# Performance work log

Measured on AMD Instinct MI355X. Metric: run time of the kernel, lower is better.

Reference implementation:

```python
import jax, jax.numpy as jnp
import numpy as np

N = 50000      # nodes
E = 1600000    # edges (avg degree 32)
D = 128        # node feature dim
C = 10         # classes
BN_EPS = 1e-5


def _w(k, shape, fan_in):
    lim = 1.0 / np.sqrt(fan_in)
    return jax.random.uniform(k, shape, jnp.float32, -lim, lim)


def setup_inputs() -> dict:
    key = jax.random.key(0)
    ks = jax.random.split(key, 16)
    inp = {}
    inp["x"] = jax.random.normal(ks[0], (N, D), jnp.float32)
    inp["edge_attr"] = jax.random.normal(ks[1], (E, 1), jnp.float32)
    inp["edge_index"] = jax.random.randint(ks[2], (2, E), 0, N)
    # edge-attr projection Linear(1, D) (D_n > D_e branch)
    inp["lin_w"] = _w(ks[3], (1, D), 1)
    inp["lin_b"] = jnp.zeros((D,), jnp.float32)
    # conv1 nn: MLP([D, D]) = Linear + ReLU + BatchNorm1d
    inp["w1"] = _w(ks[4], (D, D), D); inp["b1"] = jnp.zeros((D,)); inp["g1"] = jnp.ones((D,)); inp["be1"] = jnp.zeros((D,))
    # conv2 nn: MLP([D, 64])
    inp["w2"] = _w(ks[5], (D, 64), D); inp["b2"] = jnp.zeros((64,)); inp["g2"] = jnp.ones((64,)); inp["be2"] = jnp.zeros((64,))
    # lin1: MLP([D+64, 96])
    inp["w3"] = _w(ks[6], (D + 64, 96), D + 64); inp["b3"] = jnp.zeros((96,)); inp["g3"] = jnp.ones((96,)); inp["be3"] = jnp.zeros((96,))
    # mlp1: MLP([96, 96, C])
    inp["w4"] = _w(ks[7], (96, 96), 96); inp["b4"] = jnp.zeros((96,)); inp["g4"] = jnp.ones((96,)); inp["be4"] = jnp.zeros((96,))
    inp["w5"] = _w(ks[8], (96, C), 96); inp["b5"] = jnp.zeros((C,)); inp["g5"] = jnp.ones((C,)); inp["be5"] = jnp.zeros((C,))
    return inp


def _bn(h, g, b):
    # BatchNorm1d training-mode: batch statistics, biased variance
    m = h.mean(axis=0)
    v = h.var(axis=0)
    return g * (h - m) * jax.lax.rsqrt(v + BN_EPS) + b


def _mlp_layer(h, w, b, g, be):
    # nn.Sequential(Linear, ReLU, BatchNorm1d)
    return _bn(jax.nn.relu(h @ w + b), g, be)


def reference(x, edge_attr, edge_index, lin_w, lin_b,
              w1, b1, g1, be1, w2, b2, g2, be2,
              w3, b3, g3, be3, w4, b4, g4, be4,
              w5, b5, g5, be5):
    # project scalar edge features to node dim (D_n > D_e branch)
    e = edge_attr @ lin_w + lin_b  # [E, D]
    src, dst = edge_index[0], edge_index[1]

    def gine(h, w, b, g, be):
        # GINEConv (eps=0): nn(x_i + sum_j relu(x_j + e_ji))
        msg = jax.nn.relu(h[src] + e)                      # [E, D]
        aggr = jax.ops.segment_sum(msg, dst, num_segments=N)  # [N, D]
        return _mlp_layer(h + aggr, w, b, g, be)

    x1 = gine(x, w1, b1, g1, be1)    # [N, D]
    x2 = gine(x1, w2, b2, g2, be2)   # [N, 64]
    h = _mlp_layer(jnp.concatenate([x1, x2], axis=1), w3, b3, g3, be3)  # [N, 96]
    h = _mlp_layer(h, w4, b4, g4, be4)  # [N, 96]
    h = _mlp_layer(h, w5, b5, g5, be5)  # [N, C]
    return h
```

## Files before the change

kernel.cpp:

```cpp
#include <hip/hip_runtime.h>
#include <hip/hip_fp16.h>

static constexpr float BN_EPS = 1e-5f;

using half8 = __attribute__((ext_vector_type(8))) _Float16;
using f32x4 = __attribute__((ext_vector_type(4))) float;

__device__ __forceinline__ ushort f2h(float f) {
    return __half_as_ushort(__float2half(f));
}
__device__ __forceinline__ float2 h2f2(uint u) {
    __half2 h = *reinterpret_cast<__half2*>(&u);
    return __half22float2(h);
}
__device__ __forceinline__ float h2f1(ushort u) {
    __half h = *reinterpret_cast<__half*>(&u);
    return __half2float(h);
}

__global__ __launch_bounds__(256) void cvt_f16(
    const float* __restrict__ in, ushort* __restrict__ out, int n4)
{
    int i = blockIdx.x * 256 + threadIdx.x;
    const int stride = gridDim.x * 256;
    for (; i < n4; i += stride) {
        const float4 v = ((const float4*)in)[i];
        ushort4 u;
        u.x = f2h(v.x); u.y = f2h(v.y); u.z = f2h(v.z); u.w = f2h(v.w);
        ((ushort4*)out)[i] = u;
    }
}

__device__ __forceinline__ void pack_store(ushort* dst, int M, int k, int c, float v)
{
    const int kc = k >> 5, kk = k & 31, ct = c >> 4;
    const int lane = (c & 15) | ((kk >> 3) << 4);
    const int j = kk & 7;
    dst[((size_t)(kc * (M / 16) + ct) * 64 + lane) * 8 + j] = f2h(v);
}

__global__ __launch_bounds__(256) void pack_all(
    const float* __restrict__ w1, const float* __restrict__ w2,
    const float* __restrict__ w3, const float* __restrict__ w4,
    const float* __restrict__ w5, const float* __restrict__ b5,
    ushort* __restrict__ Wp, float* __restrict__ b5p, float* __restrict__ sums)
{
    int t = blockIdx.x * 256 + threadIdx.x;
    if (t < 16384) { pack_store(Wp, 128, t / 128, t % 128, w1[t]); return; }
    t -= 16384;
    if (t < 8192) { pack_store(Wp + 16384, 64, t / 64, t % 64, w2[t]); return; }
    t -= 8192;
    if (t < 18432) { pack_store(Wp + 24576, 96, t / 96, t % 96, w3[t]); return; }
    t -= 18432;
    if (t < 9216) { pack_store(Wp + 43008, 96, t / 96, t % 96, w4[t]); return; }
    t -= 9216;
    if (t < 1536) {
        const int k = t / 16, c = t % 16;
        pack_store(Wp + 52224, 16, k, c, (c < 10) ? w5[k * 10 + c] : 0.f);
        return;
    }
    t -= 1536;
    if (t < 16) { b5p[t] = (t < 10) ? b5[t] : 0.f; return; }
    t -= 16;
    if (t < 1280) sums[t] = 0.f;
}

__device__ inline int wave_incl_scan(int v, int lane)
{
#pragma unroll
    for (int s = 1; s < 64; s <<= 1) {
        const int t = __shfl_up(v, s, 64);
        if (lane >= s) v += t;
    }
    return v;
}

__global__ __launch_bounds__(1024) void scan1(
    const int* __restrict__ cnt, int* __restrict__ off, int* __restrict__ bsum, int n)
{
    __shared__ int wsum[16];
    const int tid = threadIdx.x, lane = tid & 63, wid = tid >> 6;
    const int i = blockIdx.x * 1024 + tid;
    const int v = (i < n) ? cnt[i] : 0;
    const int incl = wave_incl_scan(v, lane);
    if (lane == 63) wsum[wid] = incl;
    __syncthreads();
    if (wid == 0) {
        int wv = (lane < 16) ? wsum[lane] : 0;
        wv = wave_incl_scan(wv, lane);
        if (lane < 16) wsum[lane] = wv;
    }
    __syncthreads();
    const int excl = (wid > 0 ? wsum[wid - 1] : 0) + incl - v;
    if (i < n) off[i] = excl;
    if (tid == 1023) bsum[blockIdx.x] = wsum[15];
}

__global__ __launch_bounds__(64) void scan2(int* __restrict__ bsum, int nb)
{
    const int lane = threadIdx.x;
    int carry = 0;
    for (int base = 0; base < nb; base += 64) {
        const int idx = base + lane;
        const int v = (idx < nb) ? bsum[idx] : 0;
        const int incl = wave_incl_scan(v, lane);
        if (idx < nb) bsum[idx] = carry + incl - v;
        carry += __shfl(incl, 63, 64);
    }
}

__global__ __launch_bounds__(1024) void scan3(
    int* __restrict__ off, const int* __restrict__ bsum, int n)
{
    const int i = blockIdx.x * 1024 + threadIdx.x;
    if (i < n) off[i] += bsum[blockIdx.x];
}

__global__ __launch_bounds__(256) void hist_blocks(
    const int* __restrict__ dst, int* __restrict__ H, int E, int NB, int NBLK)
{
    __shared__ int h[512];
    for (int i = threadIdx.x; i < NB; i += 256) h[i] = 0;
    __syncthreads();
    const int chunk = (E + NBLK - 1) / NBLK;
    const int beg = blockIdx.x * chunk;
    const int end = min(beg + chunk, E);
    for (int i = beg + threadIdx.x; i < end; i += 256)
        atomicAdd(&h[dst[i] >> 7], 1);
    __syncthreads();
    for (int i = threadIdx.x; i < NB; i += 256)
        H[(size_t)i * NBLK + blockIdx.x] = h[i];
}

__global__ __launch_bounds__(256) void scatter_coarse(
    const int* __restrict__ src, const int* __restrict__ dst,
    const float* __restrict__ ea, const int* __restrict__ H,
    int2* __restrict__ tmp, int E, int NB, int NBLK)
{
    __shared__ int h[512];
    for (int i = threadIdx.x; i < NB; i += 256)
        h[i] = H[(size_t)i * NBLK + blockIdx.x];
    __syncthreads();
    const int chunk = (E + NBLK - 1) / NBLK;
    const int beg = blockIdx.x * chunk;
    const int end = min(beg + chunk, E);
    for (int i = beg + threadIdx.x; i < end; i += 256) {
        const int d = dst[i];
        const int pos = atomicAdd(&h[d >> 7], 1);
        tmp[pos] = make_int2(src[i] | ((d & 127) << 20), __float_as_int(ea[i]));
    }
}

__global__ __launch_bounds__(256) void fill_fine2(
    const int2* __restrict__ tmp, const int* __restrict__ H,
    int* __restrict__ off, uint* __restrict__ edges, int N, int E, int NBLK)
{
    __shared__ int cnt[128];
    __shared__ int wtot;
    const int b = blockIdx.x;
    const int base = b * 128;
    const int tid = threadIdx.x;
    const int lo = H[(size_t)b * NBLK];
    const int hi = (b + 1 < (int)gridDim.x) ? H[(size_t)(b + 1) * NBLK] : E;
    if (tid < 128) cnt[tid] = 0;
    __syncthreads();
    for (int i = lo + tid; i < hi; i += 256)
        atomicAdd(&cnt[(tmp[i].x >> 20) & 127], 1);
    __syncthreads();
    int excl = 0;
    if (tid < 128) {
        const int v = cnt[tid];
        const int incl = wave_incl_scan(v, tid & 63);
        if (tid == 63) wtot = incl;
        excl = incl - v;
    }
    __syncthreads();
    if (tid >= 64 && tid < 128) excl += wtot;
    if (tid < 128) {
        const int o = lo + excl;
        if (base + tid < N) off[base + tid] = o;
        cnt[tid] = o;
    }
    if (b == 0 && tid == 0) off[N] = E;
    __syncthreads();
    for (int i = lo + tid; i < hi; i += 256) {
        const int2 p = tmp[i];
        const int dl = (p.x >> 20) & 127;
        const int pos = atomicAdd(&cnt[dl], 1);
        edges[pos] = (uint)(p.x & 0xFFFF) | ((uint)f2h(__int_as_float(p.y)) << 16);
    }
}

template<bool AFF>
__global__ __launch_bounds__(256) void gine_aggr(
    const ushort* __restrict__ xh, const int* __restrict__ off,
    const uint* __restrict__ edges, const float* __restrict__ lw,
    const float* __restrict__ lb, const float* __restrict__ sc,
    const float* __restrict__ sh, ushort* __restrict__ outh, int N)
{
    const int q = threadIdx.x & 31;
    const int node = blockIdx.x * 8 + (threadIdx.x >> 5);
    if (node >= N) return;
    const float4 lw4 = ((const float4*)lw)[q];
    const float4 lb4 = ((const float4*)lb)[q];
    float4 sc4, sh4;
    if constexpr (AFF) {
        sc4 = ((const float4*)sc)[q];
        sh4 = ((const float4*)sh)[q];
    }
    float4 s;
    {
        const uint2 u = ((const uint2*)(xh + (size_t)node * 128))[q];
        float2 f0 = h2f2(u.x), f1 = h2f2(u.y);
        if constexpr (AFF) {
            f0.x = fmaf(f0.x, sc4.x, sh4.x); f0.y = fmaf(f0.y, sc4.y, sh4.y);
            f1.x = fmaf(f1.x, sc4.z, sh4.z); f1.y = fmaf(f1.y, sc4.w, sh4.w);
        }
        s.x = f0.x; s.y = f0.y; s.z = f1.x; s.w = f1.y;
    }

    auto acc1 = [&](uint e, uint2 u) {
        const float a = h2f1((ushort)(e >> 16));
        float2 f0 = h2f2(u.x), f1 = h2f2(u.y);
        if constexpr (AFF) {
            f0.x = fmaf(f0.x, sc4.x, sh4.x); f0.y = fmaf(f0.y, sc4.y, sh4.y);
            f1.x = fmaf(f1.x, sc4.z, sh4.z); f1.y = fmaf(f1.y, sc4.w, sh4.w);
        }
        s.x += fmaxf(fmaf(a, lw4.x, lb4.x) + f0.x, 0.f);
        s.y += fmaxf(fmaf(a, lw4.y, lb4.y) + f0.y, 0.f);
        s.z += fmaxf(fmaf(a, lw4.z, lb4.z) + f1.x, 0.f);
        s.w += fmaxf(fmaf(a, lw4.w, lb4.w) + f1.y, 0.f);
    };

    int p = off[node];
    const int pend = off[node + 1];
    for (; p + 8 <= pend; p += 8) {
        const uint e0 = edges[p + 0], e1 = edges[p + 1];
        const uint e2 = edges[p + 2], e3 = edges[p + 3];
        const uint e4 = edges[p + 4], e5 = edges[p + 5];
        const uint e6 = edges[p + 6], e7 = edges[p + 7];
        const uint2 u0 = ((const uint2*)(xh + (size_t)(e0 & 0xFFFFu) * 128))[q];
        const uint2 u1 = ((const uint2*)(xh + (size_t)(e1 & 0xFFFFu) * 128))[q];
        const uint2 u2 = ((const uint2*)(xh + (size_t)(e2 & 0xFFFFu) * 128))[q];
        const uint2 u3 = ((const uint2*)(xh + (size_t)(e3 & 0xFFFFu) * 128))[q];
        const uint2 u4 = ((const uint2*)(xh + (size_t)(e4 & 0xFFFFu) * 128))[q];
        const uint2 u5 = ((const uint2*)(xh + (size_t)(e5 & 0xFFFFu) * 128))[q];
        const uint2 u6 = ((const uint2*)(xh + (size_t)(e6 & 0xFFFFu) * 128))[q];
        const uint2 u7 = ((const uint2*)(xh + (size_t)(e7 & 0xFFFFu) * 128))[q];
        acc1(e0, u0); acc1(e1, u1); acc1(e2, u2); acc1(e3, u3);
        acc1(e4, u4); acc1(e5, u5); acc1(e6, u6); acc1(e7, u7);
    }
    for (; p < pend; ++p) {
        const uint e = edges[p];
        const uint2 u = ((const uint2*)(xh + (size_t)(e & 0xFFFFu) * 128))[q];
        acc1(e, u);
    }
    ushort4 o;
    o.x = f2h(s.x); o.y = f2h(s.y); o.z = f2h(s.z); o.w = f2h(s.w);
    ((ushort4*)(outh + (size_t)node * 128))[q] = o;
}

__device__ __forceinline__ half8 affine_h8(
    half8 a, const float* __restrict__ sc, const float* __restrict__ sh, int k)
{
    const float4 c0 = *(const float4*)(sc + k), c1 = *(const float4*)(sc + k + 4);
    const float4 d0 = *(const float4*)(sh + k), d1 = *(const float4*)(sh + k + 4);
    half8 r;
    r[0] = (_Float16)fmaf((float)a[0], c0.x, d0.x);
    r[1] = (_Float16)fmaf((float)a[1], c0.y, d0.y);
    r[2] = (_Float16)fmaf((float)a[2], c0.z, d0.z);
    r[3] = (_Float16)fmaf((float)a[3], c0.w, d0.w);
    r[4] = (_Float16)fmaf((float)a[4], c1.x, d1.x);
    r[5] = (_Float16)fmaf((float)a[5], c1.y, d1.y);
    r[6] = (_Float16)fmaf((float)a[6], c1.z, d1.z);
    r[7] = (_Float16)fmaf((float)a[7], c1.w, d1.w);
    return r;
}

template<int K, int KS, int M, bool YH, bool AF1, bool AF2>
__global__ __launch_bounds__(256) void gemm_mfma(
    const ushort* __restrict__ A1, const ushort* __restrict__ A2,
    const float* __restrict__ sc1, const float* __restrict__ sh1,
    const float* __restrict__ sc2, const float* __restrict__ sh2,
    const ushort* __restrict__ Wp, const float* __restrict__ bias,
    void* __restrict__ Yv, float* __restrict__ sum, float* __restrict__ sq, int N)
{
    constexpr int NCT = M / 16;
    constexpr int NKC = K / 32;
    __shared__ float redS[4][M];
    __shared__ float redQ[4][M];
    const int tid = threadIdx.x;
    const int w = tid >> 6, l = tid & 63;
    const int col = l & 15, kg = l >> 4;
    const int rowA = blockIdx.x * 64 + w * 16 + col;
    const int rA = (rowA < N) ? rowA : (N - 1);
    f32x4 acc[NCT];
#pragma unroll
    for (int ct = 0; ct < NCT; ++ct) acc[ct] = f32x4{0.f, 0.f, 0.f, 0.f};
#pragma unroll
    for (int kc = 0; kc < NKC; ++kc) {
        const int kbase = kc * 32 + kg * 8;
        half8 a;
        if constexpr (KS < K) {
            if (kbase >= KS) {
                a = *(const half8*)(A2 + (size_t)rA * (K - KS) + (kbase - KS));
                if constexpr (AF2) a = affine_h8(a, sc2, sh2, kbase - KS);
            } else {
                a = *(const half8*)(A1 + (size_t)rA * KS + kbase);
                if constexpr (AF1) a = affine_h8(a, sc1, sh1, kbase);
            }
        } else {
            a = *(const half8*)(A1 + (size_t)rA * K + kbase);
            if constexpr (AF1) a = affine_h8(a, sc1, sh1, kbase);
        }
#pragma unroll
        for (int ct = 0; ct < NCT; ++ct) {
            const half8 wf = *(const half8*)(Wp + ((size_t)(kc * NCT + ct) * 64 + l) * 8);
            acc[ct] = __builtin_amdgcn_mfma_f32_16x16x32_f16(a, wf, acc[ct], 0, 0, 0);
        }
    }
    const int row0 = blockIdx.x * 64 + w * 16 + 4 * kg;
#pragma unroll
    for (int ct = 0; ct < NCT; ++ct) {
        const float bs = bias[ct * 16 + col];
        float sS = 0.f, sQ = 0.f;
#pragma unroll
        for (int r = 0; r < 4; ++r) {
            const int ro = row0 + r;
            if (ro < N) {
                const float o = fmaxf(acc[ct][r] + bs, 0.f);
                if constexpr (YH) ((ushort*)Yv)[(size_t)ro * M + ct * 16 + col] = f2h(o);
                else              ((float*)Yv)[(size_t)ro * M + ct * 16 + col] = o;
                sS += o; sQ = fmaf(o, o, sQ);
            }
        }
        sS += __shfl_xor(sS, 16, 64); sQ += __shfl_xor(sQ, 16, 64);
        sS += __shfl_xor(sS, 32, 64); sQ += __shfl_xor(sQ, 32, 64);
        if (l < 16) { redS[w][ct * 16 + col] = sS; redQ[w][ct * 16 + col] = sQ; }
    }
    __syncthreads();
    for (int i = tid; i < M; i += 256) {
        const float S = redS[0][i] + redS[1][i] + redS[2][i] + redS[3][i];
        const float Q = redQ[0][i] + redQ[1][i] + redQ[2][i] + redQ[3][i];
        unsafeAtomicAdd(&sum[i], S);
        unsafeAtomicAdd(&sq[i], Q);
    }
}

template<int M>
__global__ void bn_finalize(const float* __restrict__ sum, const float* __restrict__ sq,
                            const float* __restrict__ g, const float* __restrict__ be,
                            float* __restrict__ scale, float* __restrict__ shift, float invN)
{
    const int i = threadIdx.x;
    if (i < M) {
        const float m = sum[i] * invN;
        const float v = sq[i] * invN - m * m;
        const float sc = g[i] * rsqrtf(v + BN_EPS);
        scale[i] = sc;
        shift[i] = be[i] - m * sc;
    }
}

__global__ __launch_bounds__(256) void bn_apply_final(
    const float* __restrict__ Y16, const float* __restrict__ scale,
    const float* __restrict__ shift, float* __restrict__ out, int total)
{
    for (int i = blockIdx.x * 256 + threadIdx.x; i < total; i += gridDim.x * 256) {
        const int n = i / 10;
        const int c = i - n * 10;
        out[i] = fmaf(Y16[(size_t)n * 16 + c], scale[c], shift[c]);
    }
}

extern "C" void kernel_launch(void* const* d_in, const int* in_sizes, int n_in,
                              void* d_out, int out_size, void* d_ws, size_t ws_size,
                              hipStream_t stream)
{
    const float* x   = (const float*)d_in[0];
    const float* ea  = (const float*)d_in[1];
    const int*   ei  = (const int*)d_in[2];
    const float* lw  = (const float*)d_in[3];
    const float* lb  = (const float*)d_in[4];
    const float* w1  = (const float*)d_in[5];
    const float* b1  = (const float*)d_in[6];
    const float* g1  = (const float*)d_in[7];
    const float* be1 = (const float*)d_in[8];
    const float* w2  = (const float*)d_in[9];
    const float* b2  = (const float*)d_in[10];
    const float* g2  = (const float*)d_in[11];
    const float* be2 = (const float*)d_in[12];
    const float* w3  = (const float*)d_in[13];
    const float* b3  = (const float*)d_in[14];
    const float* g3  = (const float*)d_in[15];
    const float* be3 = (const float*)d_in[16];
    const float* w4  = (const float*)d_in[17];
    const float* b4  = (const float*)d_in[18];
    const float* g4  = (const float*)d_in[19];
    const float* be4 = (const float*)d_in[20];
    const float* w5  = (const float*)d_in[21];
    const float* b5  = (const float*)d_in[22];
    const float* g5  = (const float*)d_in[23];
    const float* be5 = (const float*)d_in[24];

    const int N = in_sizes[0] / 128;
    const int E = in_sizes[1];
    const int* src = ei;
    const int* dst = ei + E;
    const float invN = 1.0f / (float)N;

    float* ws = (float*)d_ws;
    ushort* Pa = (ushort*)ws;
    ushort* Pb = (ushort*)(ws + (size_t)N * 64);
    ushort* Pc = (ushort*)(ws + (size_t)N * 128);
    ushort* Pd = (ushort*)(ws + (size_t)N * 160);
    float*  y5 = ws + (size_t)N * 208;
    float*  smallr = ws + (size_t)N * 224;
    float*  sums   = smallr;
    float*  scales = smallr + 1280;
    float*  shifts = smallr + 1920;
    float*  b5p    = smallr + 2560;
    ushort* Wp     = (ushort*)(ws + (size_t)N * 224 + 2576);
    int*    ibase  = (int*)(ws + (size_t)N * 224 + 2576 + 26880);
    int*    H      = ibase;
    int*    bsum   = H + 100160;
    int2*   tmp    = (int2*)(bsum + 128);
    uint*   edges  = (uint*)(tmp + E);
    int*    off    = (int*)(edges + E);
#define SUM(l)   (sums + (l) * 128)
#define SQ(l)    (sums + (5 + (l)) * 128)
#define SCALE(l) (scales + (l) * 128)
#define SHIFT(l) (shifts + (l) * 128)

    pack_all<<<216, 256, 0, stream>>>(w1, w2, w3, w4, w5, b5, Wp, b5p, sums);
    cvt_f16<<<2048, 256, 0, stream>>>(x, Pa, N * 32);

    const int NB   = (N + 127) / 128;
    const int NBLK = 256;
    const int nH   = NB * NBLK;
    const int nbH  = (nH + 1023) / 1024;
    hist_blocks<<<NBLK, 256, 0, stream>>>(dst, H, E, NB, NBLK);
    scan1<<<nbH, 1024, 0, stream>>>(H, H, bsum, nH);
    scan2<<<1, 64, 0, stream>>>(bsum, nbH);
    scan3<<<nbH, 1024, 0, stream>>>(H, bsum, nH);
    scatter_coarse<<<NBLK, 256, 0, stream>>>(src, dst, ea, H, tmp, E, NB, NBLK);
    fill_fine2<<<NB, 256, 0, stream>>>(tmp, H, off, edges, N, E, NBLK);

    const int gemmGrid = (N + 63) / 64;
    const int aggrGrid = (N + 7) / 8;

    gine_aggr<false><<<aggrGrid, 256, 0, stream>>>(
        Pa, off, edges, lw, lb, nullptr, nullptr, Pb, N);
    gemm_mfma<128, 128, 128, true, false, false><<<gemmGrid, 256, 0, stream>>>(
        Pb, nullptr, nullptr, nullptr, nullptr, nullptr,
        Wp, b1, Pa, SUM(0), SQ(0), N);
    bn_finalize<128><<<1, 128, 0, stream>>>(SUM(0), SQ(0), g1, be1, SCALE(0), SHIFT(0), invN);

    gine_aggr<true><<<aggrGrid, 256, 0, stream>>>(
        Pa, off, edges, lw, lb, SCALE(0), SHIFT(0), Pb, N);
    gemm_mfma<128, 128, 64, true, false, false><<<gemmGrid, 256, 0, stream>>>(
        Pb, nullptr, nullptr, nullptr, nullptr, nullptr,
        Wp + 16384, b2, Pc, SUM(1), SQ(1), N);
    bn_finalize<64><<<1, 128, 0, stream>>>(SUM(1), SQ(1), g2, be2, SCALE(1), SHIFT(1), invN);

    gemm_mfma<192, 128, 96, true, true, true><<<gemmGrid, 256, 0, stream>>>(
        Pa, Pc, SCALE(0), SHIFT(0), SCALE(1), SHIFT(1),
        Wp + 24576, b3, Pb, SUM(2), SQ(2), N);
    bn_finalize<96><<<1, 128, 0, stream>>>(SUM(2), SQ(2), g3, be3, SCALE(2), SHIFT(2), invN);

    gemm_mfma<96, 96, 96, true, true, false><<<gemmGrid, 256, 0, stream>>>(
        Pb, nullptr, SCALE(2), SHIFT(2), nullptr, nullptr,
        Wp + 43008, b4, Pd, SUM(3), SQ(3), N);
    bn_finalize<96><<<1, 128, 0, stream>>>(SUM(3), SQ(3), g4, be4, SCALE(3), SHIFT(3), invN);

    gemm_mfma<96, 96, 16, false, true, false><<<gemmGrid, 256, 0, stream>>>(
        Pd, nullptr, SCALE(3), SHIFT(3), nullptr, nullptr,
        Wp + 52224, b5p, y5, SUM(4), SQ(4), N);
    bn_finalize<10><<<1, 128, 0, stream>>>(SUM(4), SQ(4), g5, be5, SCALE(4), SHIFT(4), invN);

    bn_apply_final<<<1024, 256, 0, stream>>>(y5, SCALE(4), SHIFT(4), (float*)d_out, N * 10);
#undef SUM
#undef SQ
#undef SCALE
#undef SHIFT
}
```

Baseline: 350.2 us.

## Fuse BN finalize into consumer kernels and software-pipeline edge gather loop

```diff
diff --git a/kernel.cpp b/kernel.cpp
--- a/kernel.cpp
+++ b/kernel.cpp
@@ -195,8 +195,10 @@
 __global__ __launch_bounds__(256) void gine_aggr(
     const ushort* __restrict__ xh, const int* __restrict__ off,
     const uint* __restrict__ edges, const float* __restrict__ lw,
-    const float* __restrict__ lb, const float* __restrict__ sc,
-    const float* __restrict__ sh, ushort* __restrict__ outh, int N)
+    const float* __restrict__ lb, const float* __restrict__ su,
+    const float* __restrict__ qu, const float* __restrict__ g,
+    const float* __restrict__ be, float invN,
+    ushort* __restrict__ outh, int N)
 {
     const int q = threadIdx.x & 31;
     const int node = blockIdx.x * 8 + (threadIdx.x >> 5);
@@ -205,8 +207,18 @@
     const float4 lb4 = ((const float4*)lb)[q];
     float4 sc4, sh4;
     if constexpr (AFF) {
-        sc4 = ((const float4*)sc)[q];
-        sh4 = ((const float4*)sh)[q];
+        const float4 sv = ((const float4*)su)[q];
+        const float4 qv = ((const float4*)qu)[q];
+        const float4 gv = ((const float4*)g)[q];
+        const float4 bv = ((const float4*)be)[q];
+        float4 m;
+        m.x = sv.x * invN; m.y = sv.y * invN; m.z = sv.z * invN; m.w = sv.w * invN;
+        sc4.x = gv.x * rsqrtf(qv.x * invN - m.x * m.x + BN_EPS);
+        sc4.y = gv.y * rsqrtf(qv.y * invN - m.y * m.y + BN_EPS);
+        sc4.z = gv.z * rsqrtf(qv.z * invN - m.z * m.z + BN_EPS);
+        sc4.w = gv.w * rsqrtf(qv.w * invN - m.w * m.w + BN_EPS);
+        sh4.x = bv.x - m.x * sc4.x; sh4.y = bv.y - m.y * sc4.y;
+        sh4.z = bv.z - m.z * sc4.z; sh4.w = bv.w - m.w * sc4.w;
     }
     float4 s;
     {
@@ -218,8 +230,26 @@
         }
         s.x = f0.x; s.y = f0.y; s.z = f1.x; s.w = f1.y;
     }
-
-    auto acc1 = [&](uint e, uint2 u) {
+    int p = off[node];
+    const int pend = off[node + 1];
+    if (p < pend) {
+        uint e = edges[p];
+        uint2 u = ((const uint2*)(xh + (size_t)(e & 0xFFFFu) * 128))[q];
+        for (++p; p < pend; ++p) {
+            const uint en = edges[p];
+            const uint2 un = ((const uint2*)(xh + (size_t)(en & 0xFFFFu) * 128))[q];
+            const float a = h2f1((ushort)(e >> 16));
+            float2 f0 = h2f2(u.x), f1 = h2f2(u.y);
+            if constexpr (AFF) {
+                f0.x = fmaf(f0.x, sc4.x, sh4.x); f0.y = fmaf(f0.y, sc4.y, sh4.y);
+                f1.x = fmaf(f1.x, sc4.z, sh4.z); f1.y = fmaf(f1.y, sc4.w, sh4.w);
+            }
+            s.x += fmaxf(fmaf(a, lw4.x, lb4.x) + f0.x, 0.f);
+            s.y += fmaxf(fmaf(a, lw4.y, lb4.y) + f0.y, 0.f);
+            s.z += fmaxf(fmaf(a, lw4.z, lb4.z) + f1.x, 0.f);
+            s.w += fmaxf(fmaf(a, lw4.w, lb4.w) + f1.y, 0.f);
+            e = en; u = un;
+        }
         const float a = h2f1((ushort)(e >> 16));
         float2 f0 = h2f2(u.x), f1 = h2f2(u.y);
         if constexpr (AFF) {
@@ -230,30 +260,6 @@
         s.y += fmaxf(fmaf(a, lw4.y, lb4.y) + f0.y, 0.f);
         s.z += fmaxf(fmaf(a, lw4.z, lb4.z) + f1.x, 0.f);
         s.w += fmaxf(fmaf(a, lw4.w, lb4.w) + f1.y, 0.f);
-    };
-
-    int p = off[node];
-    const int pend = off[node + 1];
-    for (; p + 8 <= pend; p += 8) {
-        const uint e0 = edges[p + 0], e1 = edges[p + 1];
-        const uint e2 = edges[p + 2], e3 = edges[p + 3];
-        const uint e4 = edges[p + 4], e5 = edges[p + 5];
-        const uint e6 = edges[p + 6], e7 = edges[p + 7];
-        const uint2 u0 = ((const uint2*)(xh + (size_t)(e0 & 0xFFFFu) * 128))[q];
-        const uint2 u1 = ((const uint2*)(xh + (size_t)(e1 & 0xFFFFu) * 128))[q];
-        const uint2 u2 = ((const uint2*)(xh + (size_t)(e2 & 0xFFFFu) * 128))[q];
-        const uint2 u3 = ((const uint2*)(xh + (size_t)(e3 & 0xFFFFu) * 128))[q];
-        const uint2 u4 = ((const uint2*)(xh + (size_t)(e4 & 0xFFFFu) * 128))[q];
-        const uint2 u5 = ((const uint2*)(xh + (size_t)(e5 & 0xFFFFu) * 128))[q];
-        const uint2 u6 = ((const uint2*)(xh + (size_t)(e6 & 0xFFFFu) * 128))[q];
-        const uint2 u7 = ((const uint2*)(xh + (size_t)(e7 & 0xFFFFu) * 128))[q];
-        acc1(e0, u0); acc1(e1, u1); acc1(e2, u2); acc1(e3, u3);
-        acc1(e4, u4); acc1(e5, u5); acc1(e6, u6); acc1(e7, u7);
-    }
-    for (; p < pend; ++p) {
-        const uint e = edges[p];
-        const uint2 u = ((const uint2*)(xh + (size_t)(e & 0xFFFFu) * 128))[q];
-        acc1(e, u);
     }
     ushort4 o;
     o.x = f2h(s.x); o.y = f2h(s.y); o.z = f2h(s.z); o.w = f2h(s.w);
@@ -261,7 +267,7 @@
 }
 
 __device__ __forceinline__ half8 affine_h8(
-    half8 a, const float* __restrict__ sc, const float* __restrict__ sh, int k)
+    half8 a, const float* sc, const float* sh, int k)
 {
     const float4 c0 = *(const float4*)(sc + k), c1 = *(const float4*)(sc + k + 4);
     const float4 d0 = *(const float4*)(sh + k), d1 = *(const float4*)(sh + k + 4);
@@ -280,16 +286,32 @@
 template<int K, int KS, int M, bool YH, bool AF1, bool AF2>
 __global__ __launch_bounds__(256) void gemm_mfma(
     const ushort* __restrict__ A1, const ushort* __restrict__ A2,
-    const float* __restrict__ sc1, const float* __restrict__ sh1,
-    const float* __restrict__ sc2, const float* __restrict__ sh2,
+    const float* __restrict__ su1, const float* __restrict__ sq1_,
+    const float* __restrict__ g1, const float* __restrict__ be1,
+    const float* __restrict__ su2, const float* __restrict__ sq2_,
+    const float* __restrict__ g2, const float* __restrict__ be2,
     const ushort* __restrict__ Wp, const float* __restrict__ bias,
-    void* __restrict__ Yv, float* __restrict__ sum, float* __restrict__ sq, int N)
+    void* __restrict__ Yv, float* __restrict__ sum, float* __restrict__ sq,
+    int N, float invN)
 {
     constexpr int NCT = M / 16;
     constexpr int NKC = K / 32;
     __shared__ float redS[4][M];
     __shared__ float redQ[4][M];
+    __shared__ float scL[K];
+    __shared__ float shL[K];
     const int tid = threadIdx.x;
+    if constexpr (AF1 || AF2) {
+        for (int i = tid; i < K; i += 256) {
+            float s_, q_, g_, b_;
+            if (i < KS) { s_ = su1[i]; q_ = sq1_[i]; g_ = g1[i]; b_ = be1[i]; }
+            else        { s_ = su2[i - KS]; q_ = sq2_[i - KS]; g_ = g2[i - KS]; b_ = be2[i - KS]; }
+            const float m = s_ * invN;
+            const float c = g_ * rsqrtf(q_ * invN - m * m + BN_EPS);
+            scL[i] = c; shL[i] = b_ - m * c;
+        }
+        __syncthreads();
+    }
     const int w = tid >> 6, l = tid & 63;
     const int col = l & 15, kg = l >> 4;
     const int rowA = blockIdx.x * 64 + w * 16 + col;
@@ -304,14 +326,14 @@
         if constexpr (KS < K) {
             if (kbase >= KS) {
                 a = *(const half8*)(A2 + (size_t)rA * (K - KS) + (kbase - KS));
-                if constexpr (AF2) a = affine_h8(a, sc2, sh2, kbase - KS);
+                if constexpr (AF2) a = affine_h8(a, scL, shL, kbase);
             } else {
                 a = *(const half8*)(A1 + (size_t)rA * KS + kbase);
-                if constexpr (AF1) a = affine_h8(a, sc1, sh1, kbase);
+                if constexpr (AF1) a = affine_h8(a, scL, shL, kbase);
             }
         } else {
             a = *(const half8*)(A1 + (size_t)rA * K + kbase);
-            if constexpr (AF1) a = affine_h8(a, sc1, sh1, kbase);
+            if constexpr (AF1) a = affine_h8(a, scL, shL, kbase);
         }
 #pragma unroll
         for (int ct = 0; ct < NCT; ++ct) {
@@ -347,29 +369,18 @@
     }
 }
 
-template<int M>
-__global__ void bn_finalize(const float* __restrict__ sum, const float* __restrict__ sq,
-                            const float* __restrict__ g, const float* __restrict__ be,
-                            float* __restrict__ scale, float* __restrict__ shift, float invN)
-{
-    const int i = threadIdx.x;
-    if (i < M) {
-        const float m = sum[i] * invN;
-        const float v = sq[i] * invN - m * m;
-        const float sc = g[i] * rsqrtf(v + BN_EPS);
-        scale[i] = sc;
-        shift[i] = be[i] - m * sc;
-    }
-}
-
 __global__ __launch_bounds__(256) void bn_apply_final(
-    const float* __restrict__ Y16, const float* __restrict__ scale,
-    const float* __restrict__ shift, float* __restrict__ out, int total)
+    const float* __restrict__ Y16, const float* __restrict__ su,
+    const float* __restrict__ qu, const float* __restrict__ g5,
+    const float* __restrict__ be5, float* __restrict__ out, int total, float invN)
 {
     for (int i = blockIdx.x * 256 + threadIdx.x; i < total; i += gridDim.x * 256) {
         const int n = i / 10;
         const int c = i - n * 10;
-        out[i] = fmaf(Y16[(size_t)n * 16 + c], scale[c], shift[c]);
+        const float m = su[c] * invN;
+        const float sc = g5[c] * rsqrtf(qu[c] * invN - m * m + BN_EPS);
+        const float sh = be5[c] - m * sc;
+        out[i] = fmaf(Y16[(size_t)n * 16 + c], sc, sh);
     }
 }
 
@@ -417,11 +428,9 @@
     float*  y5 = ws + (size_t)N * 208;
     float*  smallr = ws + (size_t)N * 224;
     float*  sums   = smallr;
-    float*  scales = smallr + 1280;
-    float*  shifts = smallr + 1920;
-    float*  b5p    = smallr + 2560;
-    ushort* Wp     = (ushort*)(ws + (size_t)N * 224 + 2576);
-    int*    ibase  = (int*)(ws + (size_t)N * 224 + 2576 + 26880);
+    float*  b5p    = smallr + 1280;
+    ushort* Wp     = (ushort*)(ws + (size_t)N * 224 + 1296);
+    int*    ibase  = (int*)(ws + (size_t)N * 224 + 1296 + 26880);
     int*    H      = ibase;
     int*    bsum   = H + 100160;
     int2*   tmp    = (int2*)(bsum + 128);
@@ -429,8 +438,6 @@
     int*    off    = (int*)(edges + E);
 #define SUM(l)   (sums + (l) * 128)
 #define SQ(l)    (sums + (5 + (l)) * 128)
-#define SCALE(l) (scales + (l) * 128)
-#define SHIFT(l) (shifts + (l) * 128)
 
     pack_all<<<216, 256, 0, stream>>>(w1, w2, w3, w4, w5, b5, Wp, b5p, sums);
     cvt_f16<<<2048, 256, 0, stream>>>(x, Pa, N * 32);
@@ -450,37 +457,33 @@
     const int aggrGrid = (N + 7) / 8;
 
     gine_aggr<false><<<aggrGrid, 256, 0, stream>>>(
-        Pa, off, edges, lw, lb, nullptr, nullptr, Pb, N);
+        Pa, off, edges, lw, lb, nullptr, nullptr, nullptr, nullptr, invN, Pb, N);
     gemm_mfma<128, 128, 128, true, false, false><<<gemmGrid, 256, 0, stream>>>(
         Pb, nullptr, nullptr, nullptr, nullptr, nullptr,
-        Wp, b1, Pa, SUM(0), SQ(0), N);
-    bn_finalize<128><<<1, 128, 0, stream>>>(SUM(0), SQ(0), g1, be1, SCALE(0), SHIFT(0), invN);
+        nullptr, nullptr, nullptr, nullptr,
+        Wp, b1, Pa, SUM(0), SQ(0), N, invN);
 
     gine_aggr<true><<<aggrGrid, 256, 0, stream>>>(
-        Pa, off, edges, lw, lb, SCALE(0), SHIFT(0), Pb, N);
+        Pa, off, edges, lw, lb, SUM(0), SQ(0), g1, be1, invN, Pb, N);
     gemm_mfma<128, 128, 64, true, false, false><<<gemmGrid, 256, 0, stream>>>(
         Pb, nullptr, nullptr, nullptr, nullptr, nullptr,
-        Wp + 16384, b2, Pc, SUM(1), SQ(1), N);
-    bn_finalize<64><<<1, 128, 0, stream>>>(SUM(1), SQ(1), g2, be2, SCALE(1), SHIFT(1), invN);
+        nullptr, nullptr, nullptr, nullptr,
+        Wp + 16384, b2, Pc, SUM(1), SQ(1), N, invN);
 
     gemm_mfma<192, 128, 96, true, true, true><<<gemmGrid, 256, 0, stream>>>(
-        Pa, Pc, SCALE(0), SHIFT(0), SCALE(1), SHIFT(1),
-        Wp + 24576, b3, Pb, SUM(2), SQ(2), N);
-    bn_finalize<96><<<1, 128, 0, stream>>>(SUM(2), SQ(2), g3, be3, SCALE(2), SHIFT(2), invN);
+        Pa, Pc, SUM(0), SQ(0), g1, be1, SUM(1), SQ(1), g2, be2,
+        Wp + 24576, b3, Pb, SUM(2), SQ(2), N, invN);
 
     gemm_mfma<96, 96, 96, true, true, false><<<gemmGrid, 256, 0, stream>>>(
-        Pb, nullptr, SCALE(2), SHIFT(2), nullptr, nullptr,
-        Wp + 43008, b4, Pd, SUM(3), SQ(3), N);
-    bn_finalize<96><<<1, 128, 0, stream>>>(SUM(3), SQ(3), g4, be4, SCALE(3), SHIFT(3), invN);
+        Pb, nullptr, SUM(2), SQ(2), g3, be3, nullptr, nullptr, nullptr, nullptr,
+        Wp + 43008, b4, Pd, SUM(3), SQ(3), N, invN);
 
     gemm_mfma<96, 96, 16, false, true, false><<<gemmGrid, 256, 0, stream>>>(
-        Pd, nullptr, SCALE(3), SHIFT(3), nullptr, nullptr,
-        Wp + 52224, b5p, y5, SUM(4), SQ(4), N);
-    bn_finalize<10><<<1, 128, 0, stream>>>(SUM(4), SQ(4), g5, be5, SCALE(4), SHIFT(4), invN);
-
-    bn_apply_final<<<1024, 256, 0, stream>>>(y5, SCALE(4), SHIFT(4), (float*)d_out, N * 10);
+        Pd, nullptr, SUM(3), SQ(3), g4, be4, nullptr, nullptr, nullptr, nullptr,
+        Wp + 52224, b5p, y5, SUM(4), SQ(4), N, invN);
+
+    bn_apply_final<<<1024, 256, 0, stream>>>(y5, SUM(4), SQ(4), g5, be5,
+                                             (float*)d_out, N * 10, invN);
 #undef SUM
 #undef SQ
-#undef SCALE
-#undef SHIFT
-}
+}
```

Result: faster. 332.2 us (-5.1%).
